# Kernel tuning notes

Measured on AMD Instinct MI355X. Metric: run time of the kernel, lower is better.

The kernel has to match this reference:

```python
import jax, jax.numpy as jnp
import numpy as np
import math

H = 8
E = 512
D_K = E // H
NEG = -1000000000.0
# last (and only surviving) row of dist_bar: one threshold per head
DIST_BAR = np.array([0.2, 0.3, 0.4, 0.5, 0.6, 0.7, 0.8, 0.9], dtype=np.float32)


def setup_inputs() -> dict:
    key = jax.random.key(0)
    ks = jax.random.split(key, 12)
    B, N = 8, 1024
    s = 1.0 / math.sqrt(E)
    inp = {
        "query": jax.random.normal(ks[0], (B, N, E), jnp.float32),
        "key": jax.random.normal(ks[1], (B, N, E), jnp.float32),
        "value": jax.random.normal(ks[2], (B, N, E), jnp.float32),
        "dist": jax.random.uniform(ks[3], (B, 1, N, N), jnp.float32),
        "mask": jnp.ones((B, N, N), jnp.int32),
        "Wq": jax.random.normal(ks[4], (E, E), jnp.float32) * s,
        "bq": jnp.zeros((E,), jnp.float32),
        "Wk": jax.random.normal(ks[5], (E, E), jnp.float32) * s,
        "bk": jnp.zeros((E,), jnp.float32),
        "Wv": jax.random.normal(ks[6], (E, E), jnp.float32) * s,
        "bv": jnp.zeros((E,), jnp.float32),
        "Wo": jax.random.normal(ks[7], (E, E), jnp.float32) * s,
        "bo": jnp.zeros((E,), jnp.float32),
    }
    return inp


def reference(query, key, value, dist, mask, Wq, bq, Wk, bk, Wv, bv, Wo, bo):
    B, N, _ = query.shape
    # project and split heads: [B, H, N, D_K]
    def heads(x, W, b):
        return (x @ W.T + b).reshape(B, N, H, D_K).transpose(0, 2, 1, 3)
    q = heads(query, Wq, bq)
    k = heads(key, Wk, bk)
    v = heads(value, Wv, bv)
    scores = jnp.einsum("bhqd,bhkd->bhqk", q, k) / math.sqrt(D_K)
    # padding mask: [B,N,N] -> [B,1,N,N]
    scores = jnp.where(mask[:, None, :, :] == 0, NEG, scores)
    # per-head distance mask: dist [B,1,N,N] < thr[h] -> [B,H,N,N]
    thr = jnp.asarray(DIST_BAR)[None, :, None, None]
    dmask = dist < thr
    # first row/col (global atom) always attend
    dmask = dmask.at[:, :, 0, :].set(True).at[:, :, :, 0].set(True)
    scores = jnp.where(dmask, scores, NEG)
    p = jax.nn.softmax(scores, axis=-1)
    out = jnp.einsum("bhqk,bhkd->bhqd", p, v)  # [B,H,N,D_K]
    out = out.transpose(0, 2, 1, 3).reshape(B, N, H * D_K)
    return out @ Wo.T + bo
```

## Files before the change

kernel.cpp:

```cpp
#include <hip/hip_runtime.h>
#include <stdint.h>


typedef __attribute__((ext_vector_type(8))) short short8;
typedef __attribute__((ext_vector_type(4))) float floatx4;

#define MFMA16(a, b, c) __builtin_amdgcn_mfma_f32_16x16x32_bf16((a), (b), (c), 0, 0, 0)

static __device__ __forceinline__ unsigned short f2bf(float f) {
  union { float f; unsigned u; } v; v.f = f;
  unsigned r = v.u + 0x7fffu + ((v.u >> 16) & 1u);
  return (unsigned short)(r >> 16);
}

static __device__ __forceinline__ void gload_lds16(const void* g, void* l) {
  __builtin_amdgcn_global_load_lds((const __attribute__((address_space(1))) unsigned int*)g,
                                   (__attribute__((address_space(3))) unsigned int*)l,
                                   16, 0, 0);
}
static __device__ __forceinline__ int xsw(int row) { return (row & 3) ^ ((row >> 2) & 3); }

__global__ void wcast_kernel(const float* __restrict__ Wq, const float* __restrict__ Wk,
                             const float* __restrict__ Wv, const float* __restrict__ Wo,
                             unsigned short* __restrict__ o0, unsigned short* __restrict__ o1,
                             unsigned short* __restrict__ o2, unsigned short* __restrict__ o3) {
  int i = blockIdx.x * blockDim.x + threadIdx.x;
  int w = i >> 16, loc = i & 65535;
  const float* s = (w == 0) ? Wq : (w == 1) ? Wk : (w == 2) ? Wv : Wo;
  unsigned short* d = (w == 0) ? o0 : (w == 1) ? o1 : (w == 2) ? o2 : o3;
  float4 v = ((const float4*)s)[loc];
  ushort4 o;
  o.x = f2bf(v.x); o.y = f2bf(v.y); o.z = f2bf(v.z); o.w = f2bf(v.w);
  ((ushort4*)d)[loc] = o;
}

__global__ void codes_kernel(const float* __restrict__ dist, const int* __restrict__ mask,
                             unsigned char* __restrict__ codesP) {
  int t = blockIdx.x * blockDim.x + threadIdx.x;
  int flat = t << 2;
  int b = flat >> 20;
  int rem = flat & ((1 << 20) - 1);
  int row = rem >> 10;
  int col0 = rem & 1023;
  float4 d4 = ((const float4*)dist)[t];
  int4 m4 = ((const int4*)mask)[t];
  float dv[4] = {d4.x, d4.y, d4.z, d4.w};
  int mv[4] = {m4.x, m4.y, m4.z, m4.w};
  int rg = row >> 5;
  int st = (row >> 4) & 1;
  int qq = (row >> 2) & 3;
  int r = row & 3;
  size_t rowbase = (size_t)(b * 32 + rg) * 32768;
  int sub = st * 32 + r;
#pragma unroll
  for (int u = 0; u < 4; u++) {
    int col = col0 + u;
    float d = dv[u];
    int hmin = (d >= 0.2f) + (d >= 0.3f) + (d >= 0.4f) + (d >= 0.5f) +
               (d >= 0.6f) + (d >= 0.7f) + (d >= 0.8f) + (d >= 0.9f);
    unsigned char cc = (unsigned char)hmin;
    if (row == 0 || col == 0) cc = 0;
    if (mv[u] == 0) cc = 9;
    int kt = col >> 7, ci = (col >> 4) & 7, c = col & 15;
    int lane = qq * 16 + c;
    codesP[rowbase + (size_t)kt * 4096 + lane * 64 + sub + ci * 4] = cc;
  }
}

__global__ __launch_bounds__(256) void qkv_gemm(
    const float* __restrict__ Aq, const float* __restrict__ Ak, const float* __restrict__ Av,
    const unsigned short* __restrict__ Wqp, const unsigned short* __restrict__ Wkp,
    const unsigned short* __restrict__ Wvp,
    const float* __restrict__ bq, const float* __restrict__ bk, const float* __restrict__ bv,
    unsigned short* __restrict__ Qh, unsigned short* __restrict__ Kh,
    unsigned short* __restrict__ Vt) {
  const int z = blockIdx.z;
  const float* A = (z == 0) ? Aq : (z == 1) ? Ak : Av;
  const unsigned short* W = (z == 0) ? Wqp : (z == 1) ? Wkp : Wvp;
  const float* bias = (z == 0) ? bq : (z == 1) ? bk : bv;
  unsigned short* O = (z == 0) ? Qh : (z == 1) ? Kh : Vt;

  __shared__ __align__(16) short As[64 * 40];
  __shared__ __align__(16) short Bs[128 * 32];
  const int tid = threadIdx.x;
  const int lane = tid & 63;
  const int wave = tid >> 6;
  const int c = lane & 15;
  const int q = lane >> 4;
  const int m0 = blockIdx.x * 64;
  const int n0 = blockIdx.y * 128;
  const int wr = (wave >> 1) * 32;
  const int wc = (wave & 1) * 64;

  floatx4 acc[2][4];
#pragma unroll
  for (int i = 0; i < 2; i++)
#pragma unroll
    for (int j = 0; j < 4; j++) acc[i][j] = (floatx4)(0.0f);

  const int arow = tid >> 2, ach = tid & 3;
  const float* Ab = A + (size_t)(m0 + arow) * 512 + ach * 8;

  for (int k0 = 0; k0 < 512; k0 += 32) {
    __syncthreads();
#pragma unroll
    for (int it = 0; it < 2; it++) {
      int slot = wave * 128 + it * 64 + lane;
      int brow = slot >> 2, bch = slot & 3;
      int g = bch ^ xsw(brow);
      gload_lds16(W + (size_t)(n0 + brow) * 512 + k0 + g * 8,
                  &Bs[(size_t)(wave * 128 + it * 64) * 8]);
    }
    float4 a0 = *(const float4*)(Ab + k0);
    float4 a1 = *(const float4*)(Ab + k0 + 4);
    short8 av;
    av[0] = (short)f2bf(a0.x); av[1] = (short)f2bf(a0.y);
    av[2] = (short)f2bf(a0.z); av[3] = (short)f2bf(a0.w);
    av[4] = (short)f2bf(a1.x); av[5] = (short)f2bf(a1.y);
    av[6] = (short)f2bf(a1.z); av[7] = (short)f2bf(a1.w);
    *(short8*)(&As[arow * 40 + ach * 8]) = av;
    __syncthreads();

    short8 af[2], bfv[4];
#pragma unroll
    for (int i = 0; i < 2; i++)
      af[i] = *(const short8*)(&As[(wr + i * 16 + c) * 40 + q * 8]);
#pragma unroll
    for (int j = 0; j < 4; j++) {
      int row = wc + j * 16 + c;
      bfv[j] = *(const short8*)(&Bs[row * 32 + (q ^ xsw(row)) * 8]);
    }
#pragma unroll
    for (int i = 0; i < 2; i++)
#pragma unroll
      for (int j = 0; j < 4; j++)
        acc[i][j] = MFMA16(af[i], bfv[j], acc[i][j]);
  }

#pragma unroll
  for (int i = 0; i < 2; i++) {
    int gm0 = m0 + wr + i * 16 + q * 4;
#pragma unroll
    for (int j = 0; j < 4; j++) {
      int gn = n0 + wc + j * 16 + c;
      float bb = bias[gn];
      int h = gn >> 6, d = gn & 63;
      if (z == 2) {
        int b = gm0 >> 10, n = gm0 & 1023;
        ushort4 pk;
#pragma unroll
        for (int r = 0; r < 4; r++) pk[r] = f2bf(acc[i][j][r] + bb);
        *(ushort4*)(&Vt[(((size_t)(b * 8 + h) * 64 + d) << 10) + n]) = pk;
      } else {
#pragma unroll
        for (int r = 0; r < 4; r++) {
          int m = gm0 + r;
          int b = m >> 10, n = m & 1023;
          O[((((size_t)(b * 8 + h)) << 10) + n) * 64 + d] = f2bf(acc[i][j][r] + bb);
        }
      }
    }
  }
}

__global__ __launch_bounds__(256) void out_gemm(const unsigned short* __restrict__ A,
                                                const unsigned short* __restrict__ W,
                                                const float* __restrict__ bias,
                                                float* __restrict__ Out) {
  __shared__ __align__(16) short As[64 * 32];
  __shared__ __align__(16) short Bs[128 * 32];
  const int tid = threadIdx.x;
  const int lane = tid & 63;
  const int wave = tid >> 6;
  const int c = lane & 15;
  const int q = lane >> 4;
  const int m0 = blockIdx.x * 64;
  const int n0 = blockIdx.y * 128;
  const int wr = (wave >> 1) * 32;
  const int wc = (wave & 1) * 64;

  floatx4 acc[2][4];
#pragma unroll
  for (int i = 0; i < 2; i++)
#pragma unroll
    for (int j = 0; j < 4; j++) acc[i][j] = (floatx4)(0.0f);

  for (int k0 = 0; k0 < 512; k0 += 32) {
    __syncthreads();
    {
      int slot = wave * 64 + lane;
      int arow = slot >> 2, ach = slot & 3;
      int g = ach ^ xsw(arow);
      gload_lds16(A + (size_t)(m0 + arow) * 512 + k0 + g * 8, &As[(size_t)(wave * 64) * 8]);
    }
#pragma unroll
    for (int it = 0; it < 2; it++) {
      int slot = wave * 128 + it * 64 + lane;
      int brow = slot >> 2, bch = slot & 3;
      int g = bch ^ xsw(brow);
      gload_lds16(W + (size_t)(n0 + brow) * 512 + k0 + g * 8,
                  &Bs[(size_t)(wave * 128 + it * 64) * 8]);
    }
    __syncthreads();

    short8 af[2], bfv[4];
#pragma unroll
    for (int i = 0; i < 2; i++) {
      int row = wr + i * 16 + c;
      af[i] = *(const short8*)(&As[row * 32 + (q ^ xsw(row)) * 8]);
    }
#pragma unroll
    for (int j = 0; j < 4; j++) {
      int row = wc + j * 16 + c;
      bfv[j] = *(const short8*)(&Bs[row * 32 + (q ^ xsw(row)) * 8]);
    }
#pragma unroll
    for (int i = 0; i < 2; i++)
#pragma unroll
      for (int j = 0; j < 4; j++)
        acc[i][j] = MFMA16(af[i], bfv[j], acc[i][j]);
  }

#pragma unroll
  for (int i = 0; i < 2; i++) {
    int gm0 = m0 + wr + i * 16 + q * 4;
#pragma unroll
    for (int j = 0; j < 4; j++) {
      int gn = n0 + wc + j * 16 + c;
      float bb = bias[gn];
#pragma unroll
      for (int r = 0; r < 4; r++)
        Out[(size_t)(gm0 + r) * 512 + gn] = acc[i][j][r] + bb;
    }
  }
}

__global__ __launch_bounds__(256) void attn_kernel(const unsigned short* __restrict__ Qh,
                                                   const unsigned short* __restrict__ Kh,
                                                   const unsigned short* __restrict__ Vt,
                                                   const unsigned char* __restrict__ codesP,
                                                   unsigned short* __restrict__ AO) {
  __shared__ __align__(16) unsigned short P[4][32 * 132];
  const int tid = threadIdx.x;
  const int lane = tid & 63;
  const int wave = tid >> 6;
  const int c = lane & 15;
  const int q = lane >> 4;
  const int bh = blockIdx.y;
  const int b = bh >> 3;
  const int h = bh & 7;
  const size_t base = (size_t)bh << 16;
  const int rbase = blockIdx.x * 128 + wave * 32;
  const int rg = rbase >> 5;
  unsigned short* Pw = &P[wave][0];

  short8 aq[2][2];
#pragma unroll
  for (int st = 0; st < 2; st++)
#pragma unroll
    for (int kk = 0; kk < 2; kk++)
      aq[st][kk] = *(const short8*)(Qh + base + (size_t)(rbase + st * 16 + c) * 64 + kk * 32 + q * 8);

  const unsigned char* cbt = codesP + (size_t)(b * 32 + rg) * 32768 + lane * 64;
  const unsigned short* Kb = Kh + base;
  const unsigned short* Vb = Vt + base;

  float rs[2][4];
#pragma unroll
  for (int st = 0; st < 2; st++)
#pragma unroll
    for (int r = 0; r < 4; r++) rs[st][r] = 0.0f;
  floatx4 o[2][4];
#pragma unroll
  for (int st = 0; st < 2; st++)
#pragma unroll
    for (int ci = 0; ci < 4; ci++) o[st][ci] = (floatx4)(0.0f);

  for (int kt = 0; kt < 8; kt++) {
    const unsigned short* Kt = Kb + (size_t)kt * 128 * 64;
    floatx4 s[2][8];
#pragma unroll
    for (int ci = 0; ci < 8; ci++) { s[0][ci] = (floatx4)(0.0f); s[1][ci] = (floatx4)(0.0f); }
#pragma unroll
    for (int ci = 0; ci < 8; ci++)
#pragma unroll
      for (int kk = 0; kk < 2; kk++) {
        short8 bk = *(const short8*)(Kt + (size_t)(ci * 16 + c) * 64 + kk * 32 + q * 8);
        s[0][ci] = MFMA16(aq[0][kk], bk, s[0][ci]);
        s[1][ci] = MFMA16(aq[1][kk], bk, s[1][ci]);
      }
    const unsigned char* cp = cbt + (size_t)kt * 4096;
    uint4 w0 = *(const uint4*)(cp);
    uint4 w1 = *(const uint4*)(cp + 16);
    uint4 w2 = *(const uint4*)(cp + 32);
    uint4 w3 = *(const uint4*)(cp + 48);
    unsigned cv[16] = {w0.x, w0.y, w0.z, w0.w, w1.x, w1.y, w1.z, w1.w,
                       w2.x, w2.y, w2.z, w2.w, w3.x, w3.y, w3.z, w3.w};
#pragma unroll
    for (int st = 0; st < 2; st++)
#pragma unroll
      for (int ci = 0; ci < 8; ci++)
#pragma unroll
        for (int r = 0; r < 4; r++) {
          int bidx = st * 32 + ci * 4 + r;
          int code = (cv[bidx >> 2] >> ((bidx & 3) * 8)) & 0xff;
          float e = (h >= code) ? exp2f(s[st][ci][r] * 0.1803368801111362f) : 0.0f;
          rs[st][r] += e;
          Pw[(st * 16 + q * 4 + r) * 132 + ci * 16 + c] = f2bf(e);
        }
#pragma unroll
    for (int ch = 0; ch < 4; ch++) {
      short8 ap0 = *(const short8*)(&Pw[(size_t)c * 132 + ch * 32 + q * 8]);
      short8 ap1 = *(const short8*)(&Pw[(size_t)(16 + c) * 132 + ch * 32 + q * 8]);
#pragma unroll
      for (int ci = 0; ci < 4; ci++) {
        short8 bv = *(const short8*)(Vb + (size_t)(ci * 16 + c) * 1024 + kt * 128 + ch * 32 + q * 8);
        o[0][ci] = MFMA16(ap0, bv, o[0][ci]);
        o[1][ci] = MFMA16(ap1, bv, o[1][ci]);
      }
    }
  }

  float inv[2][4];
#pragma unroll
  for (int st = 0; st < 2; st++)
#pragma unroll
    for (int r = 0; r < 4; r++) {
      float v = rs[st][r];
      v += __shfl_xor(v, 1); v += __shfl_xor(v, 2);
      v += __shfl_xor(v, 4); v += __shfl_xor(v, 8);
      inv[st][r] = 1.0f / v;
    }
#pragma unroll
  for (int st = 0; st < 2; st++)
#pragma unroll
    for (int r = 0; r < 4; r++) {
      int n = rbase + st * 16 + q * 4 + r;
      size_t ob = ((size_t)((b << 10) + n)) * 512 + h * 64;
#pragma unroll
      for (int ci = 0; ci < 4; ci++)
        AO[ob + ci * 16 + c] = f2bf(o[st][ci][r] * inv[st][r]);
    }
}

extern "C" void kernel_launch(void* const* d_in, const int* in_sizes, int n_in,
                              void* d_out, int out_size, void* d_ws, size_t ws_size,
                              hipStream_t stream) {
  const float* query = (const float*)d_in[0];
  const float* key_  = (const float*)d_in[1];
  const float* value = (const float*)d_in[2];
  const float* dist  = (const float*)d_in[3];
  const int*   mask  = (const int*)d_in[4];
  const float* Wq = (const float*)d_in[5];
  const float* bq = (const float*)d_in[6];
  const float* Wk = (const float*)d_in[7];
  const float* bk = (const float*)d_in[8];
  const float* Wv = (const float*)d_in[9];
  const float* bv = (const float*)d_in[10];
  const float* Wo = (const float*)d_in[11];
  const float* bo = (const float*)d_in[12];

  char* ws = (char*)d_ws;
  size_t off = 0;
  auto alloc = [&](size_t bytes) -> char* {
    char* p = ws + off;
    off += (bytes + 255) & ~(size_t)255;
    return p;
  };
  const size_t NQKV = 8192ull * 512;
  unsigned short* wq16 = (unsigned short*)alloc(512ull * 512 * 2);
  unsigned short* wk16 = (unsigned short*)alloc(512ull * 512 * 2);
  unsigned short* wv16 = (unsigned short*)alloc(512ull * 512 * 2);
  unsigned short* wo16 = (unsigned short*)alloc(512ull * 512 * 2);
  unsigned short* Qh = (unsigned short*)alloc(NQKV * 2);
  unsigned short* Kh = (unsigned short*)alloc(NQKV * 2);
  unsigned short* Vt = (unsigned short*)alloc(NQKV * 2);
  unsigned short* AO = (unsigned short*)alloc(NQKV * 2);
  unsigned char*  codesP = (unsigned char*)alloc(8ull * 1024 * 1024);

  wcast_kernel<<<1024, 256, 0, stream>>>(Wq, Wk, Wv, Wo, wq16, wk16, wv16, wo16);
  codes_kernel<<<8192, 256, 0, stream>>>(dist, mask, codesP);
  qkv_gemm<<<dim3(128, 4, 3), 256, 0, stream>>>(query, key_, value, wq16, wk16, wv16,
                                                bq, bk, bv, Qh, Kh, Vt);
  attn_kernel<<<dim3(8, 64), 256, 0, stream>>>(Qh, Kh, Vt, codesP, AO);
  out_gemm<<<dim3(128, 4), 256, 0, stream>>>(AO, wo16, bo, (float*)d_out);
}
```

Measured before the change: 292.8 us.

## Pre-cast activations to bf16, retile GEMMs, fold Q scale, halve attention rows per wave

Casts query/key/value to bf16 in one combined cast kernel, so the QKV GEMM can stream A through async global-to-LDS loads with a swizzled layout. Both GEMMs move to 128-row M tiles, and the output GEMM uses 64-wide N tiles. The softmax scale is folded into Q in the QKV epilogue. The attention kernel processes 16 query rows per wave instead of 32 and launches twice as many blocks. This trades an extra activation read/write pass for fewer per-iteration conversions and more attention parallelism, at the cost of less K/V reuse per wave.

```diff
diff --git a/kernel.cpp b/kernel.cpp
--- a/kernel.cpp
+++ b/kernel.cpp
@@ -6,6 +6,7 @@
 typedef __attribute__((ext_vector_type(4))) float floatx4;
 
 #define MFMA16(a, b, c) __builtin_amdgcn_mfma_f32_16x16x32_bf16((a), (b), (c), 0, 0, 0)
+#define QSCALE 0.1803368801111362f
 
 static __device__ __forceinline__ unsigned short f2bf(float f) {
   union { float f; unsigned u; } v; v.f = f;
@@ -20,17 +21,28 @@
 }
 static __device__ __forceinline__ int xsw(int row) { return (row & 3) ^ ((row >> 2) & 3); }
 
-__global__ void wcast_kernel(const float* __restrict__ Wq, const float* __restrict__ Wk,
-                             const float* __restrict__ Wv, const float* __restrict__ Wo,
-                             unsigned short* __restrict__ o0, unsigned short* __restrict__ o1,
-                             unsigned short* __restrict__ o2, unsigned short* __restrict__ o3) {
+__global__ void cast_all(const float* __restrict__ q, const float* __restrict__ k,
+                         const float* __restrict__ v,
+                         const float* __restrict__ wq, const float* __restrict__ wk,
+                         const float* __restrict__ wv, const float* __restrict__ wo,
+                         unsigned short* __restrict__ qb, unsigned short* __restrict__ kb,
+                         unsigned short* __restrict__ vb,
+                         unsigned short* __restrict__ wq16, unsigned short* __restrict__ wk16,
+                         unsigned short* __restrict__ wv16, unsigned short* __restrict__ wo16) {
   int i = blockIdx.x * blockDim.x + threadIdx.x;
-  int w = i >> 16, loc = i & 65535;
-  const float* s = (w == 0) ? Wq : (w == 1) ? Wk : (w == 2) ? Wv : Wo;
-  unsigned short* d = (w == 0) ? o0 : (w == 1) ? o1 : (w == 2) ? o2 : o3;
-  float4 v = ((const float4*)s)[loc];
+  const float* s; unsigned short* d; int loc;
+  if (i < 3145728) {
+    int w = i >> 20; loc = i & 1048575;
+    s = (w == 0) ? q : (w == 1) ? k : v;
+    d = (w == 0) ? qb : (w == 1) ? kb : vb;
+  } else {
+    int j = i - 3145728; int w = j >> 16; loc = j & 65535;
+    s = (w == 0) ? wq : (w == 1) ? wk : (w == 2) ? wv : wo;
+    d = (w == 0) ? wq16 : (w == 1) ? wk16 : (w == 2) ? wv16 : wo16;
+  }
+  float4 vv = ((const float4*)s)[loc];
   ushort4 o;
-  o.x = f2bf(v.x); o.y = f2bf(v.y); o.z = f2bf(v.z); o.w = f2bf(v.w);
+  o.x = f2bf(vv.x); o.y = f2bf(vv.y); o.z = f2bf(vv.z); o.w = f2bf(vv.w);
   ((ushort4*)d)[loc] = o;
 }
 
@@ -68,77 +80,70 @@
 }
 
 __global__ __launch_bounds__(256) void qkv_gemm(
-    const float* __restrict__ Aq, const float* __restrict__ Ak, const float* __restrict__ Av,
+    const unsigned short* __restrict__ Aq, const unsigned short* __restrict__ Ak,
+    const unsigned short* __restrict__ Av,
     const unsigned short* __restrict__ Wqp, const unsigned short* __restrict__ Wkp,
     const unsigned short* __restrict__ Wvp,
     const float* __restrict__ bq, const float* __restrict__ bk, const float* __restrict__ bv,
     unsigned short* __restrict__ Qh, unsigned short* __restrict__ Kh,
     unsigned short* __restrict__ Vt) {
   const int z = blockIdx.z;
-  const float* A = (z == 0) ? Aq : (z == 1) ? Ak : Av;
+  const unsigned short* A = (z == 0) ? Aq : (z == 1) ? Ak : Av;
   const unsigned short* W = (z == 0) ? Wqp : (z == 1) ? Wkp : Wvp;
   const float* bias = (z == 0) ? bq : (z == 1) ? bk : bv;
   unsigned short* O = (z == 0) ? Qh : (z == 1) ? Kh : Vt;
 
-  __shared__ __align__(16) short As[64 * 40];
+  __shared__ __align__(16) short As[128 * 32];
   __shared__ __align__(16) short Bs[128 * 32];
   const int tid = threadIdx.x;
   const int lane = tid & 63;
   const int wave = tid >> 6;
   const int c = lane & 15;
   const int q = lane >> 4;
-  const int m0 = blockIdx.x * 64;
+  const int m0 = blockIdx.x * 128;
   const int n0 = blockIdx.y * 128;
-  const int wr = (wave >> 1) * 32;
+  const int wr = (wave >> 1) * 64;
   const int wc = (wave & 1) * 64;
 
-  floatx4 acc[2][4];
-#pragma unroll
-  for (int i = 0; i < 2; i++)
+  floatx4 acc[4][4];
+#pragma unroll
+  for (int i = 0; i < 4; i++)
 #pragma unroll
     for (int j = 0; j < 4; j++) acc[i][j] = (floatx4)(0.0f);
-
-  const int arow = tid >> 2, ach = tid & 3;
-  const float* Ab = A + (size_t)(m0 + arow) * 512 + ach * 8;
 
   for (int k0 = 0; k0 < 512; k0 += 32) {
     __syncthreads();
 #pragma unroll
     for (int it = 0; it < 2; it++) {
       int slot = wave * 128 + it * 64 + lane;
-      int brow = slot >> 2, bch = slot & 3;
-      int g = bch ^ xsw(brow);
-      gload_lds16(W + (size_t)(n0 + brow) * 512 + k0 + g * 8,
-                  &Bs[(size_t)(wave * 128 + it * 64) * 8]);
-    }
-    float4 a0 = *(const float4*)(Ab + k0);
-    float4 a1 = *(const float4*)(Ab + k0 + 4);
-    short8 av;
-    av[0] = (short)f2bf(a0.x); av[1] = (short)f2bf(a0.y);
-    av[2] = (short)f2bf(a0.z); av[3] = (short)f2bf(a0.w);
-    av[4] = (short)f2bf(a1.x); av[5] = (short)f2bf(a1.y);
-    av[6] = (short)f2bf(a1.z); av[7] = (short)f2bf(a1.w);
-    *(short8*)(&As[arow * 40 + ach * 8]) = av;
+      int row = slot >> 2, ch = slot & 3;
+      int g = ch ^ xsw(row);
+      gload_lds16(A + (size_t)(m0 + row) * 512 + k0 + g * 8, &As[(wave * 128 + it * 64) * 8]);
+      gload_lds16(W + (size_t)(n0 + row) * 512 + k0 + g * 8, &Bs[(wave * 128 + it * 64) * 8]);
+    }
     __syncthreads();
 
-    short8 af[2], bfv[4];
-#pragma unroll
-    for (int i = 0; i < 2; i++)
-      af[i] = *(const short8*)(&As[(wr + i * 16 + c) * 40 + q * 8]);
+    short8 af[4], bfv[4];
+#pragma unroll
+    for (int i = 0; i < 4; i++) {
+      int row = wr + i * 16 + c;
+      af[i] = *(const short8*)(&As[row * 32 + (q ^ xsw(row)) * 8]);
+    }
 #pragma unroll
     for (int j = 0; j < 4; j++) {
       int row = wc + j * 16 + c;
       bfv[j] = *(const short8*)(&Bs[row * 32 + (q ^ xsw(row)) * 8]);
     }
 #pragma unroll
-    for (int i = 0; i < 2; i++)
+    for (int i = 0; i < 4; i++)
 #pragma unroll
       for (int j = 0; j < 4; j++)
         acc[i][j] = MFMA16(af[i], bfv[j], acc[i][j]);
   }
 
-#pragma unroll
-  for (int i = 0; i < 2; i++) {
+  const float scale = (z == 0) ? QSCALE : 1.0f;
+#pragma unroll
+  for (int i = 0; i < 4; i++) {
     int gm0 = m0 + wr + i * 16 + q * 4;
 #pragma unroll
     for (int j = 0; j < 4; j++) {
@@ -156,7 +161,7 @@
         for (int r = 0; r < 4; r++) {
           int m = gm0 + r;
           int b = m >> 10, n = m & 1023;
-          O[((((size_t)(b * 8 + h)) << 10) + n) * 64 + d] = f2bf(acc[i][j][r] + bb);
+          O[((((size_t)(b * 8 + h)) << 10) + n) * 64 + d] = f2bf((acc[i][j][r] + bb) * scale);
         }
       }
     }
@@ -167,65 +172,64 @@
                                                 const unsigned short* __restrict__ W,
                                                 const float* __restrict__ bias,
                                                 float* __restrict__ Out) {
-  __shared__ __align__(16) short As[64 * 32];
-  __shared__ __align__(16) short Bs[128 * 32];
+  __shared__ __align__(16) short As[128 * 32];
+  __shared__ __align__(16) short Bs[64 * 32];
   const int tid = threadIdx.x;
   const int lane = tid & 63;
   const int wave = tid >> 6;
   const int c = lane & 15;
   const int q = lane >> 4;
-  const int m0 = blockIdx.x * 64;
-  const int n0 = blockIdx.y * 128;
-  const int wr = (wave >> 1) * 32;
-  const int wc = (wave & 1) * 64;
-
-  floatx4 acc[2][4];
-#pragma unroll
-  for (int i = 0; i < 2; i++)
-#pragma unroll
-    for (int j = 0; j < 4; j++) acc[i][j] = (floatx4)(0.0f);
+  const int m0 = blockIdx.x * 128;
+  const int n0 = blockIdx.y * 64;
+  const int wr = (wave >> 1) * 64;
+  const int wc = (wave & 1) * 32;
+
+  floatx4 acc[4][2];
+#pragma unroll
+  for (int i = 0; i < 4; i++)
+#pragma unroll
+    for (int j = 0; j < 2; j++) acc[i][j] = (floatx4)(0.0f);
 
   for (int k0 = 0; k0 < 512; k0 += 32) {
     __syncthreads();
+#pragma unroll
+    for (int it = 0; it < 2; it++) {
+      int slot = wave * 128 + it * 64 + lane;
+      int row = slot >> 2, ch = slot & 3;
+      int g = ch ^ xsw(row);
+      gload_lds16(A + (size_t)(m0 + row) * 512 + k0 + g * 8, &As[(wave * 128 + it * 64) * 8]);
+    }
     {
       int slot = wave * 64 + lane;
-      int arow = slot >> 2, ach = slot & 3;
-      int g = ach ^ xsw(arow);
-      gload_lds16(A + (size_t)(m0 + arow) * 512 + k0 + g * 8, &As[(size_t)(wave * 64) * 8]);
-    }
-#pragma unroll
-    for (int it = 0; it < 2; it++) {
-      int slot = wave * 128 + it * 64 + lane;
-      int brow = slot >> 2, bch = slot & 3;
-      int g = bch ^ xsw(brow);
-      gload_lds16(W + (size_t)(n0 + brow) * 512 + k0 + g * 8,
-                  &Bs[(size_t)(wave * 128 + it * 64) * 8]);
+      int row = slot >> 2, ch = slot & 3;
+      int g = ch ^ xsw(row);
+      gload_lds16(W + (size_t)(n0 + row) * 512 + k0 + g * 8, &Bs[(wave * 64) * 8]);
     }
     __syncthreads();
 
-    short8 af[2], bfv[4];
-#pragma unroll
-    for (int i = 0; i < 2; i++) {
+    short8 af[4], bfv[2];
+#pragma unroll
+    for (int i = 0; i < 4; i++) {
       int row = wr + i * 16 + c;
       af[i] = *(const short8*)(&As[row * 32 + (q ^ xsw(row)) * 8]);
     }
 #pragma unroll
-    for (int j = 0; j < 4; j++) {
+    for (int j = 0; j < 2; j++) {
       int row = wc + j * 16 + c;
       bfv[j] = *(const short8*)(&Bs[row * 32 + (q ^ xsw(row)) * 8]);
     }
 #pragma unroll
-    for (int i = 0; i < 2; i++)
-#pragma unroll
-      for (int j = 0; j < 4; j++)
+    for (int i = 0; i < 4; i++)
+#pragma unroll
+      for (int j = 0; j < 2; j++)
         acc[i][j] = MFMA16(af[i], bfv[j], acc[i][j]);
   }
 
 #pragma unroll
-  for (int i = 0; i < 2; i++) {
+  for (int i = 0; i < 4; i++) {
     int gm0 = m0 + wr + i * 16 + q * 4;
 #pragma unroll
-    for (int j = 0; j < 4; j++) {
+    for (int j = 0; j < 2; j++) {
       int gn = n0 + wc + j * 16 + c;
       float bb = bias[gn];
 #pragma unroll
@@ -240,7 +244,7 @@
                                                    const unsigned short* __restrict__ Vt,
                                                    const unsigned char* __restrict__ codesP,
                                                    unsigned short* __restrict__ AO) {
-  __shared__ __align__(16) unsigned short P[4][32 * 132];
+  __shared__ __align__(16) unsigned short P[4][16 * 132];
   const int tid = threadIdx.x;
   const int lane = tid & 63;
   const int wave = tid >> 6;
@@ -250,97 +254,77 @@
   const int b = bh >> 3;
   const int h = bh & 7;
   const size_t base = (size_t)bh << 16;
-  const int rbase = blockIdx.x * 128 + wave * 32;
+  const int rbase = blockIdx.x * 64 + wave * 16;
   const int rg = rbase >> 5;
+  const int st = (rbase >> 4) & 1;
   unsigned short* Pw = &P[wave][0];
 
-  short8 aq[2][2];
-#pragma unroll
-  for (int st = 0; st < 2; st++)
-#pragma unroll
-    for (int kk = 0; kk < 2; kk++)
-      aq[st][kk] = *(const short8*)(Qh + base + (size_t)(rbase + st * 16 + c) * 64 + kk * 32 + q * 8);
-
-  const unsigned char* cbt = codesP + (size_t)(b * 32 + rg) * 32768 + lane * 64;
+  short8 aq[2];
+#pragma unroll
+  for (int kk = 0; kk < 2; kk++)
+    aq[kk] = *(const short8*)(Qh + base + (size_t)(rbase + c) * 64 + kk * 32 + q * 8);
+
+  const unsigned char* cbt = codesP + (size_t)(b * 32 + rg) * 32768 + lane * 64 + st * 32;
   const unsigned short* Kb = Kh + base;
   const unsigned short* Vb = Vt + base;
 
-  float rs[2][4];
-#pragma unroll
-  for (int st = 0; st < 2; st++)
-#pragma unroll
-    for (int r = 0; r < 4; r++) rs[st][r] = 0.0f;
-  floatx4 o[2][4];
-#pragma unroll
-  for (int st = 0; st < 2; st++)
-#pragma unroll
-    for (int ci = 0; ci < 4; ci++) o[st][ci] = (floatx4)(0.0f);
+  float rs[4] = {0.0f, 0.0f, 0.0f, 0.0f};
+  floatx4 o[4];
+#pragma unroll
+  for (int ci = 0; ci < 4; ci++) o[ci] = (floatx4)(0.0f);
 
   for (int kt = 0; kt < 8; kt++) {
     const unsigned short* Kt = Kb + (size_t)kt * 128 * 64;
-    floatx4 s[2][8];
-#pragma unroll
-    for (int ci = 0; ci < 8; ci++) { s[0][ci] = (floatx4)(0.0f); s[1][ci] = (floatx4)(0.0f); }
+    floatx4 s[8];
+#pragma unroll
+    for (int ci = 0; ci < 8; ci++) s[ci] = (floatx4)(0.0f);
 #pragma unroll
     for (int ci = 0; ci < 8; ci++)
 #pragma unroll
       for (int kk = 0; kk < 2; kk++) {
         short8 bk = *(const short8*)(Kt + (size_t)(ci * 16 + c) * 64 + kk * 32 + q * 8);
-        s[0][ci] = MFMA16(aq[0][kk], bk, s[0][ci]);
-        s[1][ci] = MFMA16(aq[1][kk], bk, s[1][ci]);
+        s[ci] = MFMA16(aq[kk], bk, s[ci]);
       }
     const unsigned char* cp = cbt + (size_t)kt * 4096;
     uint4 w0 = *(const uint4*)(cp);
     uint4 w1 = *(const uint4*)(cp + 16);
-    uint4 w2 = *(const uint4*)(cp + 32);
-    uint4 w3 = *(const uint4*)(cp + 48);
-    unsigned cv[16] = {w0.x, w0.y, w0.z, w0.w, w1.x, w1.y, w1.z, w1.w,
-                       w2.x, w2.y, w2.z, w2.w, w3.x, w3.y, w3.z, w3.w};
-#pragma unroll
-    for (int st = 0; st < 2; st++)
-#pragma unroll
-      for (int ci = 0; ci < 8; ci++)
-#pragma unroll
-        for (int r = 0; r < 4; r++) {
-          int bidx = st * 32 + ci * 4 + r;
-          int code = (cv[bidx >> 2] >> ((bidx & 3) * 8)) & 0xff;
-          float e = (h >= code) ? exp2f(s[st][ci][r] * 0.1803368801111362f) : 0.0f;
-          rs[st][r] += e;
-          Pw[(st * 16 + q * 4 + r) * 132 + ci * 16 + c] = f2bf(e);
-        }
+    unsigned cv[8] = {w0.x, w0.y, w0.z, w0.w, w1.x, w1.y, w1.z, w1.w};
+#pragma unroll
+    for (int ci = 0; ci < 8; ci++)
+#pragma unroll
+      for (int r = 0; r < 4; r++) {
+        int code = (cv[ci] >> (r * 8)) & 0xff;
+        float e = (h >= code) ? exp2f(s[ci][r]) : 0.0f;
+        rs[r] += e;
+        Pw[(q * 4 + r) * 132 + ci * 16 + c] = f2bf(e);
+      }
 #pragma unroll
     for (int ch = 0; ch < 4; ch++) {
-      short8 ap0 = *(const short8*)(&Pw[(size_t)c * 132 + ch * 32 + q * 8]);
-      short8 ap1 = *(const short8*)(&Pw[(size_t)(16 + c) * 132 + ch * 32 + q * 8]);
+      short8 ap = *(const short8*)(&Pw[(size_t)c * 132 + ch * 32 + q * 8]);
 #pragma unroll
       for (int ci = 0; ci < 4; ci++) {
         short8 bv = *(const short8*)(Vb + (size_t)(ci * 16 + c) * 1024 + kt * 128 + ch * 32 + q * 8);
-        o[0][ci] = MFMA16(ap0, bv, o[0][ci]);
-        o[1][ci] = MFMA16(ap1, bv, o[1][ci]);
+        o[ci] = MFMA16(ap, bv, o[ci]);
       }
     }
   }
 
-  float inv[2][4];
-#pragma unroll
-  for (int st = 0; st < 2; st++)
-#pragma unroll
-    for (int r = 0; r < 4; r++) {
-      float v = rs[st][r];
-      v += __shfl_xor(v, 1); v += __shfl_xor(v, 2);
-      v += __shfl_xor(v, 4); v += __shfl_xor(v, 8);
-      inv[st][r] = 1.0f / v;
-    }
-#pragma unroll
-  for (int st = 0; st < 2; st++)
-#pragma unroll
-    for (int r = 0; r < 4; r++) {
-      int n = rbase + st * 16 + q * 4 + r;
-      size_t ob = ((size_t)((b << 10) + n)) * 512 + h * 64;
-#pragma unroll
-      for (int ci = 0; ci < 4; ci++)
-        AO[ob + ci * 16 + c] = f2bf(o[st][ci][r] * inv[st][r]);
-    }
+  float inv[4];
+#pragma unroll
+  for (int r = 0; r < 4; r++) {
+    float v = rs[r];
+    v += __shfl_xor(v, 1); v += __shfl_xor(v, 2);
+    v += __shfl_xor(v, 4); v += __shfl_xor(v, 8);
+    inv[r] = 1.0f / v;
+  }
+#pragma unroll
+  for (int r = 0; r < 4; r++) {
+    int n = rbase + q * 4 + r;
+    size_t ob = ((size_t)((b << 10) + n)) * 512 + h * 64;
+#pragma unroll
+    for (int ci = 0; ci < 4; ci++)
+      AO[ob + ci * 16 + c] = f2bf(o[ci][r] * inv[r]);
+  }
 }
 
 extern "C" void kernel_launch(void* const* d_in, const int* in_sizes, int n_in,
@@ -368,6 +352,9 @@
     return p;
   };
   const size_t NQKV = 8192ull * 512;
+  unsigned short* qb   = (unsigned short*)alloc(NQKV * 2);
+  unsigned short* kb   = (unsigned short*)alloc(NQKV * 2);
+  unsigned short* vb   = (unsigned short*)alloc(NQKV * 2);
   unsigned short* wq16 = (unsigned short*)alloc(512ull * 512 * 2);
   unsigned short* wk16 = (unsigned short*)alloc(512ull * 512 * 2);
   unsigned short* wv16 = (unsigned short*)alloc(512ull * 512 * 2);
@@ -378,10 +365,11 @@
   unsigned short* AO = (unsigned short*)alloc(NQKV * 2);
   unsigned char*  codesP = (unsigned char*)alloc(8ull * 1024 * 1024);
 
-  wcast_kernel<<<1024, 256, 0, stream>>>(Wq, Wk, Wv, Wo, wq16, wk16, wv16, wo16);
+  cast_all<<<13312, 256, 0, stream>>>(query, key_, value, Wq, Wk, Wv, Wo,
+                                      qb, kb, vb, wq16, wk16, wv16, wo16);
   codes_kernel<<<8192, 256, 0, stream>>>(dist, mask, codesP);
-  qkv_gemm<<<dim3(128, 4, 3), 256, 0, stream>>>(query, key_, value, wq16, wk16, wv16,
-                                                bq, bk, bv, Qh, Kh, Vt);
-  attn_kernel<<<dim3(8, 64), 256, 0, stream>>>(Qh, Kh, Vt, codesP, AO);
-  out_gemm<<<dim3(128, 4), 256, 0, stream>>>(AO, wo16, bo, (float*)d_out);
-}
+  qkv_gemm<<<dim3(64, 4, 3), 256, 0, stream>>>(qb, kb, vb, wq16, wk16, wv16,
+                                               bq, bk, bv, Qh, Kh, Vt);
+  attn_kernel<<<dim3(16, 64), 256, 0, stream>>>(Qh, Kh, Vt, codesP, AO);
+  out_gemm<<<dim3(64, 8), 256, 0, stream>>>(AO, wo16, bo, (float*)d_out);
+}
```

Result: slower. 332.8 us (+13.7%).
